# Kernel optimization log

Measured on AMD Instinct MI355X. Metric: run time of the kernel, lower is better.

Reference implementation:

```python
import jax, jax.numpy as jnp
import numpy as np
from jax import lax

HEADS = 8
HD = 96          # head_dim = dim // num_heads
DIM = HEADS * HD # 768
EPS = 1e-5
STRIDE_Q = (1, 2, 2)
STRIDE_KV = (1, 2, 2)


def _layernorm(x, w, b):
    m = jnp.mean(x, axis=-1, keepdims=True)
    v = jnp.mean(jnp.square(x - m), axis=-1, keepdims=True)
    return (x - m) * lax.rsqrt(v + EPS) * w + b


def _attention_pool(ten, conv_w, ln_w, ln_b, thw, stride):
    # ten: [B, heads, 1+L, hd]; norm is LayerNorm -> no BN/GELU branch.
    B, nH, _, C = ten.shape
    T, H, W = thw
    cls_tok, rest = ten[:, :, :1, :], ten[:, :, 1:, :]
    r = rest.reshape(B * nH, T, H, W, C).transpose(0, 4, 1, 2, 3)  # NCDHW
    r = lax.conv_general_dilated(
        r, conv_w, window_strides=stride, padding=[(1, 1)] * 3,
        dimension_numbers=("NCDHW", "OIDHW", "NCDHW"),
        feature_group_count=C)  # depthwise Conv3d, bias=False
    Tp, Hp, Wp = r.shape[2], r.shape[3], r.shape[4]
    r = r.reshape(B, nH, C, Tp * Hp * Wp).transpose(0, 1, 3, 2)
    out = jnp.concatenate([cls_tok, r], axis=2)
    out = _layernorm(out, ln_w, ln_b)  # LayerNorm(head_dim) applied incl. cls
    return out, (Tp, Hp, Wp)


def setup_inputs() -> dict:
    key = jax.random.key(0)
    ks = jax.random.split(key, 12)
    B, T, H, W = 8, 8, 28, 28
    N = 1 + T * H * W
    s = 0.02
    inp = {
        "x": jax.random.normal(ks[0], (B, N, DIM), jnp.float32),
        "qkv_w": jax.random.normal(ks[1], (3 * DIM, DIM), jnp.float32) * s,
        "pool_q_w": jax.random.normal(ks[2], (HD, 1, 3, 3, 3), jnp.float32) * s,
        "pool_k_w": jax.random.normal(ks[3], (HD, 1, 3, 3, 3), jnp.float32) * s,
        "pool_v_w": jax.random.normal(ks[4], (HD, 1, 3, 3, 3), jnp.float32) * s,
        "nq_w": jnp.ones((HD,), jnp.float32),
        "nq_b": jnp.zeros((HD,), jnp.float32),
        "nk_w": jnp.ones((HD,), jnp.float32),
        "nk_b": jnp.zeros((HD,), jnp.float32),
        "nv_w": jnp.ones((HD,), jnp.float32),
        "nv_b": jnp.zeros((HD,), jnp.float32),
        "proj_w": jax.random.normal(ks[5], (DIM, DIM), jnp.float32) * s,
        "proj_b": jnp.zeros((DIM,), jnp.float32),
        "t": T, "h": H, "w": W,
    }
    return inp


def reference(x, qkv_w, pool_q_w, pool_k_w, pool_v_w, nq_w, nq_b, nk_w, nk_b,
              nv_w, nv_b, proj_w, proj_b, t, h, w):
    B, N, C = x.shape
    scale = HD ** -0.5
    qkv = (x @ qkv_w.T).reshape(B, N, 3, HEADS, HD).transpose(2, 0, 3, 1, 4)
    q, k, v = qkv[0], qkv[1], qkv[2]  # [B, heads, N, hd]
    thw = (t, h, w)
    q, q_shape = _attention_pool(q, pool_q_w, nq_w, nq_b, thw, STRIDE_Q)
    k, _ = _attention_pool(k, pool_k_w, nk_w, nk_b, thw, STRIDE_KV)
    v, _ = _attention_pool(v, pool_v_w, nv_w, nv_b, thw, STRIDE_KV)
    attn = jnp.einsum("bhqd,bhkd->bhqk", q * scale, k)
    attn = jax.nn.softmax(attn, axis=-1)
    out = jnp.einsum("bhqk,bhkd->bhqd", attn, v) + q  # residual q add
    Nq = out.shape[2]
    out = out.transpose(0, 2, 1, 3).reshape(B, Nq, C)
    out = out @ proj_w.T + proj_b
    return out
```

## Files before the change

kernel.cpp:

```cpp
#include <hip/hip_runtime.h>
#include <hip/hip_bf16.h>

typedef short s16x8 __attribute__((ext_vector_type(8)));
typedef float f32x4 __attribute__((ext_vector_type(4)));

#define DEVI __device__ __forceinline__

DEVI unsigned short f2bf(float f) {
  unsigned u = __builtin_bit_cast(unsigned, f);
  u += 0x7FFFu + ((u >> 16) & 1u);
  return (unsigned short)(u >> 16);
}
DEVI float bf2f(unsigned short h) {
  unsigned u = ((unsigned)h) << 16;
  return __builtin_bit_cast(float, u);
}

DEVI void gload_lds16(const void* g, void* l) {
  __builtin_amdgcn_global_load_lds((const __attribute__((address_space(1))) void*)g,
                                   (__attribute__((address_space(3))) void*)l, 16, 0, 0);
}

__global__ void cvt_f2b(const float* __restrict__ src, unsigned short* __restrict__ dst, int n4) {
  int i = blockIdx.x * blockDim.x + threadIdx.x;
  if (i < n4) {
    float4 v = ((const float4*)src)[i];
    ushort4 o;
    o.x = f2bf(v.x); o.y = f2bf(v.y); o.z = f2bf(v.z); o.w = f2bf(v.w);
    ((ushort4*)dst)[i] = o;
  }
}

template <int MODE>
__global__ __launch_bounds__(256) void gemm_bf16(
    const unsigned short* __restrict__ A, const unsigned short* __restrict__ B,
    int M, int Nmat, int K, int Ntok,
    unsigned short* __restrict__ Oq, unsigned short* __restrict__ Ok, unsigned short* __restrict__ Ov,
    const float* __restrict__ bias, float* __restrict__ Cout) {
  __shared__ unsigned short As[128 * 32];
  __shared__ unsigned short Bs[128 * 32];
  const int tid = threadIdx.x;
  const int wave = tid >> 6, lane = tid & 63;
  const int tm = blockIdx.x, tn = blockIdx.y;
  const int wr = wave >> 1, wc = wave & 1;
  const int sr = lane >> 2;
  const int sc = (lane & 3) * 8;
  const int l15 = lane & 15, lg = lane >> 4;
  f32x4 acc[4][4] = {};

  for (int kt = 0; kt < K; kt += 32) {
    #pragma unroll
    for (int i = 0; i < 2; ++i) {
      int r = wave * 32 + i * 16 + sr;
      long ar = (long)tm * 128 + r; if (ar >= M) ar = M - 1;
      long br = (long)tn * 128 + r; if (br >= Nmat) br = Nmat - 1;
      gload_lds16(A + ar * K + kt + sc, &As[(wave * 32 + i * 16) * 32]);
      gload_lds16(B + br * K + kt + sc, &Bs[(wave * 32 + i * 16) * 32]);
    }
    asm volatile("s_waitcnt vmcnt(0)" ::: "memory");
    __syncthreads();
    s16x8 a[4], bfr[4];
    #pragma unroll
    for (int m = 0; m < 4; ++m)
      a[m] = *(const s16x8*)&As[(wr * 64 + m * 16 + l15) * 32 + lg * 8];
    #pragma unroll
    for (int n = 0; n < 4; ++n)
      bfr[n] = *(const s16x8*)&Bs[(wc * 64 + n * 16 + l15) * 32 + lg * 8];
    #pragma unroll
    for (int m = 0; m < 4; ++m)
      #pragma unroll
      for (int n = 0; n < 4; ++n)
        acc[m][n] = __builtin_amdgcn_mfma_f32_16x16x32_bf16(a[m], bfr[n], acc[m][n], 0, 0, 0);
    __syncthreads();
  }

  const long rbase = (long)tm * 128 + wr * 64 + lg * 4;
  const int cbase = tn * 128 + wc * 64 + l15;
  #pragma unroll
  for (int m = 0; m < 4; ++m)
    #pragma unroll
    for (int n = 0; n < 4; ++n)
      #pragma unroll
      for (int reg = 0; reg < 4; ++reg) {
        long gr = rbase + m * 16 + reg;
        int gc = cbase + n * 16;
        if (gr < M) {
          float c = acc[m][n][reg];
          if (MODE == 0) {
            int which = gc / 768; int rem = gc - which * 768;
            int head = rem / 96;  int d = rem - head * 96;
            int b = (int)(gr / Ntok); int tok = (int)(gr - (long)b * Ntok);
            unsigned short* dst = (which == 0) ? Oq : (which == 1) ? Ok : Ov;
            dst[((long)(b * 8 + head) * Ntok + tok) * 96 + d] = f2bf(c);
          } else {
            Cout[gr * (long)Nmat + gc] = c + bias[gc];
          }
        }
      }
}

__global__ __launch_bounds__(384) void pool_ln(
    const unsigned short* __restrict__ src, const float* __restrict__ cw,
    const float* __restrict__ lw, const float* __restrict__ lb,
    unsigned short* __restrict__ dstb, float* __restrict__ dstf) {
  const int c = threadIdx.x;
  const int r = threadIdx.y;
  const int pair = blockIdx.y;
  const int p = blockIdx.x * 4 + r;
  __shared__ float red[4][128][2];
  float val = 0.f;
  const bool active = (p < 1569);
  if (active) {
    if (p == 0) {
      val = bf2f(src[((long)pair * 6273) * 96 + c]);
    } else {
      const int q = p - 1;
      const int tp = q / 196, rem = q - tp * 196;
      const int hp = rem / 14, wp = rem - hp * 14;
      const float* w = cw + c * 27;
      float s = 0.f;
      #pragma unroll
      for (int dt = 0; dt < 3; ++dt) {
        int t = tp + dt - 1;
        if (t < 0 || t >= 8) continue;
        #pragma unroll
        for (int dh = 0; dh < 3; ++dh) {
          int hh = hp * 2 + dh - 1;
          if (hh < 0 || hh >= 28) continue;
          #pragma unroll
          for (int dw = 0; dw < 3; ++dw) {
            int ww = wp * 2 + dw - 1;
            if (ww < 0 || ww >= 28) continue;
            s += bf2f(src[((long)pair * 6273 + 1 + (t * 28 + hh) * 28 + ww) * 96 + c]) * w[dt * 9 + dh * 3 + dw];
          }
        }
      }
      val = s;
    }
  }
  red[r][c][0] = active ? val : 0.f;
  red[r][c][1] = active ? val * val : 0.f;
  if (c < 32) { red[r][96 + c][0] = 0.f; red[r][96 + c][1] = 0.f; }
  __syncthreads();
  for (int s2 = 64; s2 > 0; s2 >>= 1) {
    if (c < s2) {
      red[r][c][0] += red[r][c + s2][0];
      red[r][c][1] += red[r][c + s2][1];
    }
    __syncthreads();
  }
  if (active) {
    const float mean = red[r][0][0] * (1.f / 96.f);
    const float var = red[r][0][1] * (1.f / 96.f) - mean * mean;
    const float nv = (val - mean) * rsqrtf(var + 1e-5f) * lw[c] + lb[c];
    const long o = ((long)pair * 1569 + p) * 96 + c;
    dstb[o] = f2bf(nv);
    if (dstf) dstf[o] = nv;
  }
}

__global__ __launch_bounds__(256) void flash_attn(
    const unsigned short* __restrict__ Qb, const unsigned short* __restrict__ Kb,
    const unsigned short* __restrict__ Vb, const float* __restrict__ Qf,
    unsigned short* __restrict__ Out) {
  const int Np = 1569;
  const int pair = blockIdx.y;
  const int b = pair >> 3, h = pair & 7;
  const int tid = threadIdx.x, wave = tid >> 6, lane = tid & 63;
  const int l15 = lane & 15, lg = lane >> 4;
  const int qbase = blockIdx.x * 64 + wave * 16;
  __shared__ unsigned short Ks[32][104];
  __shared__ unsigned short Vt[96][40];
  __shared__ unsigned short Ps[4][16][40];

  s16x8 qf[3];
  {
    int qr = qbase + l15; if (qr >= Np) qr = Np - 1;
    const unsigned short* qp = &Qb[((long)pair * Np + qr) * 96];
    qf[0] = *(const s16x8*)(qp + 0  + lg * 8);
    qf[1] = *(const s16x8*)(qp + 32 + lg * 8);
    qf[2] = *(const s16x8*)(qp + 64 + lg * 8);
  }
  f32x4 accO[6] = {};
  float mrun[4], lrun[4];
  #pragma unroll
  for (int i = 0; i < 4; ++i) { mrun[i] = -1e30f; lrun[i] = 0.f; }

  const float scale = 0.1020620726159658f;
  const int NT = (Np + 31) / 32;
  for (int kt = 0; kt < NT; ++kt) {
    __syncthreads();
    for (int cc = tid; cc < 384; cc += 256) {
      int key = cc / 12, dp = (cc - key * 12) * 8;
      int gk = kt * 32 + key;
      s16x8 kv = {0,0,0,0,0,0,0,0}, vv = {0,0,0,0,0,0,0,0};
      if (gk < Np) {
        kv = *(const s16x8*)&Kb[((long)pair * Np + gk) * 96 + dp];
        vv = *(const s16x8*)&Vb[((long)pair * Np + gk) * 96 + dp];
      }
      *(s16x8*)&Ks[key][dp] = kv;
      #pragma unroll
      for (int j = 0; j < 8; ++j) Vt[dp + j][key] = (unsigned short)vv[j];
    }
    __syncthreads();

    f32x4 s0 = {}, s1 = {};
    #pragma unroll
    for (int kk = 0; kk < 3; ++kk) {
      s16x8 b0 = *(const s16x8*)&Ks[l15][kk * 32 + lg * 8];
      s16x8 b1 = *(const s16x8*)&Ks[16 + l15][kk * 32 + lg * 8];
      s0 = __builtin_amdgcn_mfma_f32_16x16x32_bf16(qf[kk], b0, s0, 0, 0, 0);
      s1 = __builtin_amdgcn_mfma_f32_16x16x32_bf16(qf[kk], b1, s1, 0, 0, 0);
    }

    const bool v0 = (kt * 32 + l15) < Np;
    const bool v1 = (kt * 32 + 16 + l15) < Np;
    float sf[4];
    #pragma unroll
    for (int i2 = 0; i2 < 4; ++i2) {
      float sm0 = v0 ? s0[i2] * scale : -1e30f;
      float sm1 = v1 ? s1[i2] * scale : -1e30f;
      float t = fmaxf(sm0, sm1);
      t = fmaxf(t, __shfl_xor(t, 1, 16));
      t = fmaxf(t, __shfl_xor(t, 2, 16));
      t = fmaxf(t, __shfl_xor(t, 4, 16));
      t = fmaxf(t, __shfl_xor(t, 8, 16));
      float mnew = fmaxf(mrun[i2], t);
      sf[i2] = __expf(mrun[i2] - mnew);
      mrun[i2] = mnew;
      float p0 = __expf(sm0 - mnew);
      float p1 = __expf(sm1 - mnew);
      float ps = p0 + p1;
      ps += __shfl_xor(ps, 1, 16);
      ps += __shfl_xor(ps, 2, 16);
      ps += __shfl_xor(ps, 4, 16);
      ps += __shfl_xor(ps, 8, 16);
      lrun[i2] = lrun[i2] * sf[i2] + ps;
      Ps[wave][lg * 4 + i2][l15] = f2bf(p0);
      Ps[wave][lg * 4 + i2][16 + l15] = f2bf(p1);
    }
    #pragma unroll
    for (int db = 0; db < 6; ++db)
      #pragma unroll
      for (int i2 = 0; i2 < 4; ++i2)
        accO[db][i2] *= sf[i2];
    asm volatile("s_waitcnt lgkmcnt(0)" ::: "memory");
    __builtin_amdgcn_sched_barrier(0);
    s16x8 ap = *(const s16x8*)&Ps[wave][l15][lg * 8];
    #pragma unroll
    for (int db = 0; db < 6; ++db) {
      s16x8 bv = *(const s16x8*)&Vt[db * 16 + l15][lg * 8];
      accO[db] = __builtin_amdgcn_mfma_f32_16x16x32_bf16(ap, bv, accO[db], 0, 0, 0);
    }
  }

  #pragma unroll
  for (int i2 = 0; i2 < 4; ++i2) lrun[i2] = 1.f / lrun[i2];
  const int q0 = qbase + lg * 4;
  #pragma unroll
  for (int db = 0; db < 6; ++db) {
    int d = db * 16 + l15;
    #pragma unroll
    for (int i2 = 0; i2 < 4; ++i2) {
      int q = q0 + i2;
      if (q < Np) {
        float o = accO[db][i2] * lrun[i2] + Qf[((long)pair * Np + q) * 96 + d];
        Out[((long)b * Np + q) * 768 + h * 96 + d] = f2bf(o);
      }
    }
  }
}

extern "C" void kernel_launch(void* const* d_in, const int* in_sizes, int n_in,
                              void* d_out, int out_size, void* d_ws, size_t ws_size,
                              hipStream_t stream) {
  const float* x     = (const float*)d_in[0];
  const float* qkv_w = (const float*)d_in[1];
  const float* pqw   = (const float*)d_in[2];
  const float* pkw   = (const float*)d_in[3];
  const float* pvw   = (const float*)d_in[4];
  const float* nqw   = (const float*)d_in[5];
  const float* nqb   = (const float*)d_in[6];
  const float* nkw   = (const float*)d_in[7];
  const float* nkb   = (const float*)d_in[8];
  const float* nvw   = (const float*)d_in[9];
  const float* nvb   = (const float*)d_in[10];
  const float* pw    = (const float*)d_in[11];
  const float* pb    = (const float*)d_in[12];

  const int Ntok = 6273, DIM = 768, Np = 1569;
  const long Mq = 8L * Ntok;
  const long Mp = 8L * Np;

  char* w = (char*)d_ws;
  unsigned short* xb  = (unsigned short*)w; w += Mq * DIM * 2;
  unsigned short* wb  = (unsigned short*)w; w += 3L * DIM * DIM * 2;
  unsigned short* pwb = (unsigned short*)w; w += (long)DIM * DIM * 2;
  unsigned short* qb  = (unsigned short*)w; w += 64L * Ntok * 96 * 2;
  unsigned short* kb  = (unsigned short*)w; w += 64L * Ntok * 96 * 2;
  unsigned short* vb  = (unsigned short*)w; w += 64L * Ntok * 96 * 2;
  unsigned short* qpb = (unsigned short*)w; w += 64L * Np * 96 * 2;
  unsigned short* kpb = (unsigned short*)w; w += 64L * Np * 96 * 2;
  unsigned short* vpb = (unsigned short*)w; w += 64L * Np * 96 * 2;
  float*          qpf = (float*)w;          w += 64L * Np * 96 * 4;
  unsigned short* ares= (unsigned short*)w; w += Mp * DIM * 2;

  {
    int n4 = (int)(Mq * DIM / 4);
    cvt_f2b<<<(n4 + 255) / 256, 256, 0, stream>>>(x, xb, n4);
    n4 = 3 * DIM * DIM / 4;
    cvt_f2b<<<(n4 + 255) / 256, 256, 0, stream>>>(qkv_w, wb, n4);
    n4 = DIM * DIM / 4;
    cvt_f2b<<<(n4 + 255) / 256, 256, 0, stream>>>(pw, pwb, n4);
  }
  {
    dim3 g((unsigned)((Mq + 127) / 128), (unsigned)((3 * DIM) / 128));
    gemm_bf16<0><<<g, 256, 0, stream>>>(xb, wb, (int)Mq, 3 * DIM, DIM, Ntok,
                                        qb, kb, vb, nullptr, nullptr);
  }
  {
    dim3 g((unsigned)((Np + 3) / 4), 64);
    dim3 blk(96, 4);
    pool_ln<<<g, blk, 0, stream>>>(qb, pqw, nqw, nqb, qpb, qpf);
    pool_ln<<<g, blk, 0, stream>>>(kb, pkw, nkw, nkb, kpb, nullptr);
    pool_ln<<<g, blk, 0, stream>>>(vb, pvw, nvw, nvb, vpb, nullptr);
  }
  {
    dim3 g((unsigned)((Np + 63) / 64), 64);
    flash_attn<<<g, 256, 0, stream>>>(qpb, kpb, vpb, qpf, ares);
  }
  {
    dim3 g((unsigned)((Mp + 127) / 128), (unsigned)(DIM / 128));
    gemm_bf16<1><<<g, 256, 0, stream>>>(ares, pwb, (int)Mp, DIM, DIM, 0,
                                        nullptr, nullptr, nullptr, pb, (float*)d_out);
  }
}
```

Before: 1.897 ms.

## Pre-transpose pooled V, warp-shuffle LayerNorm, and double query tile per wave in attention

The pool+LayerNorm kernel now gives each row to 32 lanes handling 3 channels each and reduces with warp shuffles, replacing the shared-memory tree with its many barriers. The V variant writes its output transposed into a padded [d][1600] layout, so flash attention can load V tiles with vector loads instead of scattered LDS transposes. Flash attention now processes 32 queries per wave (128 per block), so each K/V tile is reused across two MFMA row tiles. It also swizzles the P scratch to avoid LDS bank conflicts, orders the grid pair-major, and clamps out-of-range keys. The cost is higher register pressure, padded V workspace, and an extra barrier in the V pooling kernel.

```diff
diff --git a/kernel.cpp b/kernel.cpp
--- a/kernel.cpp
+++ b/kernel.cpp
@@ -99,173 +99,220 @@
       }
 }
 
-__global__ __launch_bounds__(384) void pool_ln(
+template <int MODE>
+__global__ __launch_bounds__(256) void pool_ln2(
     const unsigned short* __restrict__ src, const float* __restrict__ cw,
     const float* __restrict__ lw, const float* __restrict__ lb,
-    unsigned short* __restrict__ dstb, float* __restrict__ dstf) {
-  const int c = threadIdx.x;
-  const int r = threadIdx.y;
-  const int pair = blockIdx.y;
-  const int p = blockIdx.x * 4 + r;
-  __shared__ float red[4][128][2];
-  float val = 0.f;
-  const bool active = (p < 1569);
-  if (active) {
+    unsigned short* __restrict__ dst, float* __restrict__ dstf) {
+  __shared__ unsigned short vt[8][96];
+  const int tid = threadIdx.x;
+  const int pair = blockIdx.x;
+  const int slot = tid >> 5;
+  const int lane5 = tid & 31;
+  const int p = blockIdx.y * 8 + slot;
+  const bool valid = (p < 1569);
+
+  if (MODE != 2 && !valid) return;
+
+  float val[3] = {0.f, 0.f, 0.f};
+  if (valid) {
     if (p == 0) {
-      val = bf2f(src[((long)pair * 6273) * 96 + c]);
+      #pragma unroll
+      for (int j = 0; j < 3; ++j)
+        val[j] = bf2f(src[(long)pair * 6273 * 96 + lane5 + 32 * j]);
     } else {
       const int q = p - 1;
       const int tp = q / 196, rem = q - tp * 196;
       const int hp = rem / 14, wp = rem - hp * 14;
-      const float* w = cw + c * 27;
-      float s = 0.f;
       #pragma unroll
       for (int dt = 0; dt < 3; ++dt) {
         int t = tp + dt - 1;
-        if (t < 0 || t >= 8) continue;
+        if ((unsigned)t >= 8u) continue;
         #pragma unroll
         for (int dh = 0; dh < 3; ++dh) {
           int hh = hp * 2 + dh - 1;
-          if (hh < 0 || hh >= 28) continue;
+          if ((unsigned)hh >= 28u) continue;
           #pragma unroll
           for (int dw = 0; dw < 3; ++dw) {
             int ww = wp * 2 + dw - 1;
-            if (ww < 0 || ww >= 28) continue;
-            s += bf2f(src[((long)pair * 6273 + 1 + (t * 28 + hh) * 28 + ww) * 96 + c]) * w[dt * 9 + dh * 3 + dw];
+            if ((unsigned)ww >= 28u) continue;
+            const unsigned short* sp = src + ((long)pair * 6273 + 1 + (t * 28 + hh) * 28 + ww) * 96;
+            const int widx = dt * 9 + dh * 3 + dw;
+            #pragma unroll
+            for (int j = 0; j < 3; ++j) {
+              int c = lane5 + 32 * j;
+              val[j] += bf2f(sp[c]) * cw[c * 27 + widx];
+            }
           }
         }
       }
-      val = s;
-    }
-  }
-  red[r][c][0] = active ? val : 0.f;
-  red[r][c][1] = active ? val * val : 0.f;
-  if (c < 32) { red[r][96 + c][0] = 0.f; red[r][96 + c][1] = 0.f; }
-  __syncthreads();
-  for (int s2 = 64; s2 > 0; s2 >>= 1) {
-    if (c < s2) {
-      red[r][c][0] += red[r][c + s2][0];
-      red[r][c][1] += red[r][c + s2][1];
-    }
-    __syncthreads();
-  }
-  if (active) {
-    const float mean = red[r][0][0] * (1.f / 96.f);
-    const float var = red[r][0][1] * (1.f / 96.f) - mean * mean;
-    const float nv = (val - mean) * rsqrtf(var + 1e-5f) * lw[c] + lb[c];
-    const long o = ((long)pair * 1569 + p) * 96 + c;
-    dstb[o] = f2bf(nv);
-    if (dstf) dstf[o] = nv;
+    }
+  }
+  float s1 = val[0] + val[1] + val[2];
+  float s2 = val[0] * val[0] + val[1] * val[1] + val[2] * val[2];
+  #pragma unroll
+  for (int k = 1; k < 32; k <<= 1) {
+    s1 += __shfl_xor(s1, k, 32);
+    s2 += __shfl_xor(s2, k, 32);
+  }
+  const float mean = s1 * (1.f / 96.f);
+  const float var = s2 * (1.f / 96.f) - mean * mean;
+  const float rstd = rsqrtf(var + 1e-5f);
+  if (MODE == 2) {
+    #pragma unroll
+    for (int j = 0; j < 3; ++j) {
+      int c = lane5 + 32 * j;
+      float nv = valid ? ((val[j] - mean) * rstd * lw[c] + lb[c]) : 0.f;
+      vt[slot][c] = f2bf(nv);
+    }
+    __syncthreads();
+    if (tid < 96) {
+      s16x8 o;
+      #pragma unroll
+      for (int s = 0; s < 8; ++s) o[s] = (short)vt[s][tid];
+      *(s16x8*)&dst[(long)pair * 153600 + (long)tid * 1600 + blockIdx.y * 8] = o;
+    }
+  } else {
+    #pragma unroll
+    for (int j = 0; j < 3; ++j) {
+      int c = lane5 + 32 * j;
+      float nv = (val[j] - mean) * rstd * lw[c] + lb[c];
+      long off = ((long)pair * 1569 + p) * 96 + c;
+      dst[off] = f2bf(nv);
+      if (MODE == 0) dstf[off] = nv;
+    }
   }
 }
 
 __global__ __launch_bounds__(256) void flash_attn(
     const unsigned short* __restrict__ Qb, const unsigned short* __restrict__ Kb,
-    const unsigned short* __restrict__ Vb, const float* __restrict__ Qf,
+    const unsigned short* __restrict__ VtG, const float* __restrict__ Qf,
     unsigned short* __restrict__ Out) {
   const int Np = 1569;
-  const int pair = blockIdx.y;
+  const int pair = blockIdx.x;
   const int b = pair >> 3, h = pair & 7;
   const int tid = threadIdx.x, wave = tid >> 6, lane = tid & 63;
   const int l15 = lane & 15, lg = lane >> 4;
-  const int qbase = blockIdx.x * 64 + wave * 16;
-  __shared__ unsigned short Ks[32][104];
-  __shared__ unsigned short Vt[96][40];
-  __shared__ unsigned short Ps[4][16][40];
-
-  s16x8 qf[3];
-  {
-    int qr = qbase + l15; if (qr >= Np) qr = Np - 1;
-    const unsigned short* qp = &Qb[((long)pair * Np + qr) * 96];
-    qf[0] = *(const s16x8*)(qp + 0  + lg * 8);
-    qf[1] = *(const s16x8*)(qp + 32 + lg * 8);
-    qf[2] = *(const s16x8*)(qp + 64 + lg * 8);
-  }
-  f32x4 accO[6] = {};
-  float mrun[4], lrun[4];
-  #pragma unroll
-  for (int i = 0; i < 4; ++i) { mrun[i] = -1e30f; lrun[i] = 0.f; }
+  const int qbase = blockIdx.y * 128 + wave * 32;
+
+  __shared__ unsigned short Ks[32 * 104];
+  __shared__ unsigned short Vs[96 * 40];
+  __shared__ unsigned short Ps[4 * 32 * 40];
+
+  s16x8 qf[2][3];
+  #pragma unroll
+  for (int m = 0; m < 2; ++m) {
+    int qr = qbase + m * 16 + l15; if (qr >= Np) qr = Np - 1;
+    const unsigned short* qp = &Qb[((long)pair * Np + qr) * 96 + lg * 8];
+    qf[m][0] = *(const s16x8*)(qp);
+    qf[m][1] = *(const s16x8*)(qp + 32);
+    qf[m][2] = *(const s16x8*)(qp + 64);
+  }
+
+  f32x4 accO[2][6] = {};
+  float mrun[2][4], lrun[2][4], sf[2][4];
+  #pragma unroll
+  for (int m = 0; m < 2; ++m)
+    #pragma unroll
+    for (int i = 0; i < 4; ++i) { mrun[m][i] = -1e30f; lrun[m][i] = 0.f; }
 
   const float scale = 0.1020620726159658f;
-  const int NT = (Np + 31) / 32;
+  const int NT = 50;
+  const long kvbase = (long)pair * Np;
+  const long vbase = (long)pair * 153600;
+
   for (int kt = 0; kt < NT; ++kt) {
     __syncthreads();
     for (int cc = tid; cc < 384; cc += 256) {
       int key = cc / 12, dp = (cc - key * 12) * 8;
-      int gk = kt * 32 + key;
-      s16x8 kv = {0,0,0,0,0,0,0,0}, vv = {0,0,0,0,0,0,0,0};
-      if (gk < Np) {
-        kv = *(const s16x8*)&Kb[((long)pair * Np + gk) * 96 + dp];
-        vv = *(const s16x8*)&Vb[((long)pair * Np + gk) * 96 + dp];
-      }
-      *(s16x8*)&Ks[key][dp] = kv;
-      #pragma unroll
-      for (int j = 0; j < 8; ++j) Vt[dp + j][key] = (unsigned short)vv[j];
-    }
-    __syncthreads();
-
-    f32x4 s0 = {}, s1 = {};
+      int gk = kt * 32 + key; if (gk >= Np) gk = Np - 1;
+      s16x8 kv = *(const s16x8*)&Kb[(kvbase + gk) * 96 + dp];
+      *(s16x8*)&Ks[key * 104 + dp] = kv;
+    }
+    for (int cc = tid; cc < 384; cc += 256) {
+      int row = cc >> 2, coff = (cc & 3) * 8;
+      s16x8 vv = *(const s16x8*)&VtG[vbase + (long)row * 1600 + kt * 32 + coff];
+      *(s16x8*)&Vs[row * 40 + coff] = vv;
+    }
+    __syncthreads();
+
+    f32x4 s[2][2] = {};
     #pragma unroll
     for (int kk = 0; kk < 3; ++kk) {
-      s16x8 b0 = *(const s16x8*)&Ks[l15][kk * 32 + lg * 8];
-      s16x8 b1 = *(const s16x8*)&Ks[16 + l15][kk * 32 + lg * 8];
-      s0 = __builtin_amdgcn_mfma_f32_16x16x32_bf16(qf[kk], b0, s0, 0, 0, 0);
-      s1 = __builtin_amdgcn_mfma_f32_16x16x32_bf16(qf[kk], b1, s1, 0, 0, 0);
+      s16x8 b0 = *(const s16x8*)&Ks[l15 * 104 + kk * 32 + lg * 8];
+      s16x8 b1 = *(const s16x8*)&Ks[(16 + l15) * 104 + kk * 32 + lg * 8];
+      #pragma unroll
+      for (int m = 0; m < 2; ++m) {
+        s[m][0] = __builtin_amdgcn_mfma_f32_16x16x32_bf16(qf[m][kk], b0, s[m][0], 0, 0, 0);
+        s[m][1] = __builtin_amdgcn_mfma_f32_16x16x32_bf16(qf[m][kk], b1, s[m][1], 0, 0, 0);
+      }
     }
 
     const bool v0 = (kt * 32 + l15) < Np;
     const bool v1 = (kt * 32 + 16 + l15) < Np;
-    float sf[4];
-    #pragma unroll
-    for (int i2 = 0; i2 < 4; ++i2) {
-      float sm0 = v0 ? s0[i2] * scale : -1e30f;
-      float sm1 = v1 ? s1[i2] * scale : -1e30f;
-      float t = fmaxf(sm0, sm1);
-      t = fmaxf(t, __shfl_xor(t, 1, 16));
-      t = fmaxf(t, __shfl_xor(t, 2, 16));
-      t = fmaxf(t, __shfl_xor(t, 4, 16));
-      t = fmaxf(t, __shfl_xor(t, 8, 16));
-      float mnew = fmaxf(mrun[i2], t);
-      sf[i2] = __expf(mrun[i2] - mnew);
-      mrun[i2] = mnew;
-      float p0 = __expf(sm0 - mnew);
-      float p1 = __expf(sm1 - mnew);
-      float ps = p0 + p1;
-      ps += __shfl_xor(ps, 1, 16);
-      ps += __shfl_xor(ps, 2, 16);
-      ps += __shfl_xor(ps, 4, 16);
-      ps += __shfl_xor(ps, 8, 16);
-      lrun[i2] = lrun[i2] * sf[i2] + ps;
-      Ps[wave][lg * 4 + i2][l15] = f2bf(p0);
-      Ps[wave][lg * 4 + i2][16 + l15] = f2bf(p1);
-    }
-    #pragma unroll
-    for (int db = 0; db < 6; ++db)
-      #pragma unroll
-      for (int i2 = 0; i2 < 4; ++i2)
-        accO[db][i2] *= sf[i2];
-    asm volatile("s_waitcnt lgkmcnt(0)" ::: "memory");
-    __builtin_amdgcn_sched_barrier(0);
-    s16x8 ap = *(const s16x8*)&Ps[wave][l15][lg * 8];
+    #pragma unroll
+    for (int m = 0; m < 2; ++m)
+      #pragma unroll
+      for (int i2 = 0; i2 < 4; ++i2) {
+        float sm0 = v0 ? s[m][0][i2] * scale : -1e30f;
+        float sm1 = v1 ? s[m][1][i2] * scale : -1e30f;
+        float t = fmaxf(sm0, sm1);
+        t = fmaxf(t, __shfl_xor(t, 1, 16));
+        t = fmaxf(t, __shfl_xor(t, 2, 16));
+        t = fmaxf(t, __shfl_xor(t, 4, 16));
+        t = fmaxf(t, __shfl_xor(t, 8, 16));
+        float mnew = fmaxf(mrun[m][i2], t);
+        sf[m][i2] = __expf(mrun[m][i2] - mnew);
+        mrun[m][i2] = mnew;
+        float p0 = __expf(sm0 - mnew);
+        float p1 = __expf(sm1 - mnew);
+        float ps = p0 + p1;
+        ps += __shfl_xor(ps, 1, 16);
+        ps += __shfl_xor(ps, 2, 16);
+        ps += __shfl_xor(ps, 4, 16);
+        ps += __shfl_xor(ps, 8, 16);
+        lrun[m][i2] = lrun[m][i2] * sf[m][i2] + ps;
+        const int row = m * 16 + lg * 4 + i2;
+        Ps[wave * 1280 + row * 40 + (((l15 >> 3) ^ lg) << 3) + (l15 & 7)] = f2bf(p0);
+        Ps[wave * 1280 + row * 40 + ((((16 + l15) >> 3) ^ lg) << 3) + (l15 & 7)] = f2bf(p1);
+      }
+    #pragma unroll
+    for (int m = 0; m < 2; ++m)
+      #pragma unroll
+      for (int db = 0; db < 6; ++db)
+        #pragma unroll
+        for (int i2 = 0; i2 < 4; ++i2)
+          accO[m][db][i2] *= sf[m][i2];
+
+    s16x8 ap[2];
+    #pragma unroll
+    for (int m = 0; m < 2; ++m)
+      ap[m] = *(const s16x8*)&Ps[wave * 1280 + (m * 16 + l15) * 40 + ((lg ^ ((l15 >> 2) & 3)) << 3)];
     #pragma unroll
     for (int db = 0; db < 6; ++db) {
-      s16x8 bv = *(const s16x8*)&Vt[db * 16 + l15][lg * 8];
-      accO[db] = __builtin_amdgcn_mfma_f32_16x16x32_bf16(ap, bv, accO[db], 0, 0, 0);
-    }
-  }
-
-  #pragma unroll
-  for (int i2 = 0; i2 < 4; ++i2) lrun[i2] = 1.f / lrun[i2];
-  const int q0 = qbase + lg * 4;
-  #pragma unroll
-  for (int db = 0; db < 6; ++db) {
-    int d = db * 16 + l15;
-    #pragma unroll
-    for (int i2 = 0; i2 < 4; ++i2) {
-      int q = q0 + i2;
-      if (q < Np) {
-        float o = accO[db][i2] * lrun[i2] + Qf[((long)pair * Np + q) * 96 + d];
-        Out[((long)b * Np + q) * 768 + h * 96 + d] = f2bf(o);
+      s16x8 bv = *(const s16x8*)&Vs[(db * 16 + l15) * 40 + lg * 8];
+      accO[0][db] = __builtin_amdgcn_mfma_f32_16x16x32_bf16(ap[0], bv, accO[0][db], 0, 0, 0);
+      accO[1][db] = __builtin_amdgcn_mfma_f32_16x16x32_bf16(ap[1], bv, accO[1][db], 0, 0, 0);
+    }
+  }
+
+  #pragma unroll
+  for (int m = 0; m < 2; ++m)
+    #pragma unroll
+    for (int i2 = 0; i2 < 4; ++i2) lrun[m][i2] = 1.f / lrun[m][i2];
+  #pragma unroll
+  for (int m = 0; m < 2; ++m) {
+    const int q0 = qbase + m * 16 + lg * 4;
+    #pragma unroll
+    for (int db = 0; db < 6; ++db) {
+      int d = db * 16 + l15;
+      #pragma unroll
+      for (int i2 = 0; i2 < 4; ++i2) {
+        int q = q0 + i2;
+        if (q < Np) {
+          float o = accO[m][db][i2] * lrun[m][i2] + Qf[((long)pair * Np + q) * 96 + d];
+          Out[((long)b * Np + q) * 768 + h * 96 + d] = f2bf(o);
+        }
       }
     }
   }
@@ -301,7 +348,7 @@
   unsigned short* vb  = (unsigned short*)w; w += 64L * Ntok * 96 * 2;
   unsigned short* qpb = (unsigned short*)w; w += 64L * Np * 96 * 2;
   unsigned short* kpb = (unsigned short*)w; w += 64L * Np * 96 * 2;
-  unsigned short* vpb = (unsigned short*)w; w += 64L * Np * 96 * 2;
+  unsigned short* vpt = (unsigned short*)w; w += 64L * 96 * 1600 * 2;
   float*          qpf = (float*)w;          w += 64L * Np * 96 * 4;
   unsigned short* ares= (unsigned short*)w; w += Mp * DIM * 2;
 
@@ -319,15 +366,15 @@
                                         qb, kb, vb, nullptr, nullptr);
   }
   {
-    dim3 g((unsigned)((Np + 3) / 4), 64);
-    dim3 blk(96, 4);
-    pool_ln<<<g, blk, 0, stream>>>(qb, pqw, nqw, nqb, qpb, qpf);
-    pool_ln<<<g, blk, 0, stream>>>(kb, pkw, nkw, nkb, kpb, nullptr);
-    pool_ln<<<g, blk, 0, stream>>>(vb, pvw, nvw, nvb, vpb, nullptr);
-  }
-  {
-    dim3 g((unsigned)((Np + 63) / 64), 64);
-    flash_attn<<<g, 256, 0, stream>>>(qpb, kpb, vpb, qpf, ares);
+    dim3 gq(64, (unsigned)((Np + 7) / 8));
+    dim3 gv(64, 200);
+    pool_ln2<0><<<gq, 256, 0, stream>>>(qb, pqw, nqw, nqb, qpb, qpf);
+    pool_ln2<1><<<gq, 256, 0, stream>>>(kb, pkw, nkw, nkb, kpb, nullptr);
+    pool_ln2<2><<<gv, 256, 0, stream>>>(vb, pvw, nvw, nvb, vpt, nullptr);
+  }
+  {
+    dim3 g(64, (unsigned)((Np + 127) / 128));
+    flash_attn<<<g, 256, 0, stream>>>(qpb, kpb, vpt, qpf, ares);
   }
   {
     dim3 g((unsigned)((Mp + 127) / 128), (unsigned)(DIM / 128));
```

After: 1.728 ms. -8.9%, faster.
